# Optimization experiments

Hardware: AMD Instinct MI355X
Metric: run time of the kernel (lower is better)

Reference implementation:

```python
import math
import jax, jax.numpy as jnp
import numpy as np

N_HEADS = 16
D_EMBED = 1024
D_HEAD = D_EMBED // N_HEADS
B, S = 4, 2048


def setup_inputs() -> dict:
    key = jax.random.key(0)
    k1, k2, k3, k4, k5 = jax.random.split(key, 5)
    scale_in = 1.0 / math.sqrt(D_EMBED)
    return {
        "x": jax.random.normal(k1, (B, S, D_EMBED), dtype=jnp.float32),
        "w_in": jax.random.normal(k2, (3 * D_EMBED, D_EMBED), dtype=jnp.float32) * scale_in,
        "b_in": jax.random.normal(k3, (3 * D_EMBED,), dtype=jnp.float32) * 0.02,
        "w_out": jax.random.normal(k4, (D_EMBED, D_EMBED), dtype=jnp.float32) * scale_in,
        "b_out": jax.random.normal(k5, (D_EMBED,), dtype=jnp.float32) * 0.02,
        "causal_mask": 1,
    }


def reference(x, w_in, b_in, w_out, b_out, causal_mask):
    Bn, Sn, D = x.shape
    # fused QKV projection (torch Linear: x @ W.T + b)
    qkv = x @ w_in.T + b_in                       # (B, S, 3D)
    q, k, v = jnp.split(qkv, 3, axis=-1)
    def to_heads(t):
        return t.reshape(Bn, Sn, N_HEADS, D_HEAD).transpose(0, 2, 1, 3)  # (B,H,S,dh)
    q, k, v = to_heads(q), to_heads(k), to_heads(v)
    # manual scaled dot-product attention, full (B,H,S,S) scores
    scores = jnp.einsum("bhqd,bhkd->bhqk", q, k)
    if causal_mask:
        tri = jnp.triu(jnp.ones((Sn, Sn), dtype=bool), k=1)
        scores = jnp.where(tri, -jnp.inf, scores)
    scores = scores / math.sqrt(D_HEAD)
    weights = jax.nn.softmax(scores, axis=-1)
    out = jnp.einsum("bhqk,bhkd->bhqd", weights, v)  # (B,H,S,dh)
    out = out.transpose(0, 2, 1, 3).reshape(Bn, Sn, D)
    return out @ w_out.T + b_out
```

## Files before the change

### kernel.cpp

```cpp
#include <hip/hip_runtime.h>

typedef __bf16 bf16x8 __attribute__((ext_vector_type(8)));
typedef float  f32x4  __attribute__((ext_vector_type(4)));
typedef unsigned int uint;

__device__ inline unsigned short f2bf(float f) {
  union { float f; unsigned int u; } v; v.f = f;
  unsigned int u = v.u;
  unsigned int r = u + 0x7FFF + ((u >> 16) & 1);
  return (unsigned short)(r >> 16);
}

__device__ inline void load_lds16(const unsigned short* g, unsigned short* l) {
  __builtin_amdgcn_global_load_lds(
      (const __attribute__((address_space(1))) uint*)(g),
      (__attribute__((address_space(3))) uint*)(l), 16, 0, 0);
}

__global__ void cvt_f32_bf16(const float* __restrict__ in,
                             unsigned short* __restrict__ out, int n) {
  int i = (blockIdx.x * blockDim.x + threadIdx.x) * 4;
  if (i + 3 < n) {
    float4 f = *reinterpret_cast<const float4*>(in + i);
    ushort4 o;
    o.x = f2bf(f.x); o.y = f2bf(f.y); o.z = f2bf(f.z); o.w = f2bf(f.w);
    *reinterpret_cast<ushort4*>(out + i) = o;
  } else {
    for (; i < n; ++i) out[i] = f2bf(in[i]);
  }
}

template<bool OUT_BF16>
__global__ __launch_bounds__(256) void gemm_bt128(
    const unsigned short* __restrict__ A,
    const unsigned short* __restrict__ B,
    const float* __restrict__ bias,
    void* __restrict__ Cout,
    int M, int N, int K, int ldc)
{
  __shared__ __attribute__((aligned(16))) unsigned short As[128 * 64];
  __shared__ __attribute__((aligned(16))) unsigned short Bs[128 * 64];

  const int t    = threadIdx.x;
  const int wave = t >> 6, lane = t & 63;
  const int l16  = lane & 15, quad = lane >> 4;
  const int wr = wave >> 1, wc = wave & 1;
  const int m0 = blockIdx.y * 128, n0 = blockIdx.x * 128;

  f32x4 acc[4][4] = {};

  for (int k0 = 0; k0 < K; k0 += 64) {
#pragma unroll
    for (int i = 0; i < 4; ++i) {
      int chunk = i * 256 + t;
      int row = chunk >> 3, col = (chunk & 7) * 8;
      load_lds16(A + (size_t)(m0 + row) * K + k0 + col, As + chunk * 8);
    }
#pragma unroll
    for (int i = 0; i < 4; ++i) {
      int chunk = i * 256 + t;
      int row = chunk >> 3, col = (chunk & 7) * 8;
      load_lds16(B + (size_t)(n0 + row) * K + k0 + col, Bs + chunk * 8);
    }
    __syncthreads();
#pragma unroll
    for (int ks = 0; ks < 2; ++ks) {
      bf16x8 af[4], bfr[4];
#pragma unroll
      for (int mt = 0; mt < 4; ++mt)
        af[mt] = *(const bf16x8*)(As + (wr * 64 + mt * 16 + l16) * 64 + ks * 32 + quad * 8);
#pragma unroll
      for (int nt = 0; nt < 4; ++nt)
        bfr[nt] = *(const bf16x8*)(Bs + (wc * 64 + nt * 16 + l16) * 64 + ks * 32 + quad * 8);
#pragma unroll
      for (int mt = 0; mt < 4; ++mt)
#pragma unroll
        for (int nt = 0; nt < 4; ++nt)
          acc[mt][nt] = __builtin_amdgcn_mfma_f32_16x16x32_bf16(af[mt], bfr[nt], acc[mt][nt], 0, 0, 0);
    }
    __syncthreads();
  }

#pragma unroll
  for (int nt = 0; nt < 4; ++nt) {
    int col = n0 + wc * 64 + nt * 16 + l16;
    float bv = bias[col];
#pragma unroll
    for (int mt = 0; mt < 4; ++mt) {
#pragma unroll
      for (int r = 0; r < 4; ++r) {
        int row = m0 + wr * 64 + mt * 16 + quad * 4 + r;
        float v = acc[mt][nt][r] + bv;
        if (OUT_BF16)
          ((unsigned short*)Cout)[(size_t)row * ldc + col] = f2bf(v);
        else
          ((float*)Cout)[(size_t)row * ldc + col] = v;
      }
    }
  }
}

__global__ __launch_bounds__(256) void attn(
    const unsigned short* __restrict__ qkv,
    unsigned short* __restrict__ y,
    const int* __restrict__ flag)
{
  __shared__ __attribute__((aligned(16))) unsigned short Qs[64][72];
  __shared__ __attribute__((aligned(16))) unsigned short Ks[64][72];
  __shared__ __attribute__((aligned(16))) unsigned short VtF[64 * 64];
  __shared__ __attribute__((aligned(16))) unsigned short Ps[64][72];

  const int t    = threadIdx.x;
  const int wave = t >> 6, lane = t & 63;
  const int l16  = lane & 15, quad = lane >> 4;
  const int idx = blockIdx.x;
  const int bh  = idx & 63;
  const int qt  = 31 - (idx >> 6);
  const int b = bh >> 4, h = bh & 15;
  const int causal = flag[0];
  const int q0 = qt * 64;

  const unsigned short* Qg = qkv + (size_t)b * 2048 * 3072 + h * 64;
  const unsigned short* Kg = Qg + 1024;
  const unsigned short* Vg = Qg + 2048;

  {
    int r = t >> 2, c = (t & 3) * 16;
    const unsigned short* src = Qg + (size_t)(q0 + r) * 3072 + c;
    *(uint4*)&Qs[r][c]     = *(const uint4*)src;
    *(uint4*)&Qs[r][c + 8] = *(const uint4*)(src + 8);
  }
  __syncthreads();

  bf16x8 qf[2];
  qf[0] = *(const bf16x8*)&Qs[wave * 16 + l16][quad * 8];
  qf[1] = *(const bf16x8*)&Qs[wave * 16 + l16][32 + quad * 8];

  f32x4 ot[4] = {};
  float l_lane = 0.f;

  const float SCALE = 0.18033688011112042f;
  const int q_glob = q0 + wave * 16 + l16;
  const int jmax = causal ? qt : 31;

  for (int j = 0; j <= jmax; ++j) {
    const int kv0 = j * 64;
    {
      int r = t >> 2, c = (t & 3) * 16;
      const unsigned short* src = Kg + (size_t)(kv0 + r) * 3072 + c;
      *(uint4*)&Ks[r][c]     = *(const uint4*)src;
      *(uint4*)&Ks[r][c + 8] = *(const uint4*)(src + 8);
    }
    {
      int r = t >> 3;
      int c = (t & 7) * 8;
      int g = t & 7;
#pragma unroll
      for (int rr = 0; rr < 64; rr += 32) {
        int kv = r + rr;
        int bk = kv >> 3;
        uint4 vv = *(const uint4*)(Vg + (size_t)(kv0 + kv) * 3072 + c);
        const unsigned short* vs = (const unsigned short*)&vv;
        int base = ((bk ^ g) << 3) + (kv & 7);
#pragma unroll
        for (int i = 0; i < 8; ++i)
          VtF[(c + i) * 64 + base] = vs[i];
      }
    }
    __syncthreads();

    f32x4 st[4] = {};
#pragma unroll
    for (int ks = 0; ks < 2; ++ks) {
#pragma unroll
      for (int mt = 0; mt < 4; ++mt) {
        bf16x8 kf = *(const bf16x8*)&Ks[mt * 16 + l16][ks * 32 + quad * 8];
        st[mt] = __builtin_amdgcn_mfma_f32_16x16x32_bf16(kf, qf[ks], st[mt], 0, 0, 0);
      }
    }

    const bool diag = (causal != 0) && (j == jmax);
#pragma unroll
    for (int mt = 0; mt < 4; ++mt) {
      float p[4];
#pragma unroll
      for (int r = 0; r < 4; ++r) {
        float pv = __builtin_amdgcn_exp2f(st[mt][r] * SCALE);
        if (diag) {
          int kv = kv0 + mt * 16 + quad * 4 + r;
          if (kv > q_glob) pv = 0.f;
        }
        p[r] = pv;
        l_lane += pv;
      }
      uint2 w;
      w.x = (uint)f2bf(p[0]) | ((uint)f2bf(p[1]) << 16);
      w.y = (uint)f2bf(p[2]) | ((uint)f2bf(p[3]) << 16);
      *(uint2*)&Ps[wave * 16 + l16][mt * 16 + quad * 4] = w;
    }
    __threadfence_block();

#pragma unroll
    for (int ks = 0; ks < 2; ++ks) {
      bf16x8 pf = *(const bf16x8*)&Ps[wave * 16 + l16][ks * 32 + quad * 8];
#pragma unroll
      for (int mt = 0; mt < 4; ++mt) {
        int d = mt * 16 + l16;
        int g = (d >> 3) & 7;
        bf16x8 vf = *(const bf16x8*)(VtF + d * 64 + (((ks * 4 + quad) ^ g) << 3));
        ot[mt] = __builtin_amdgcn_mfma_f32_16x16x32_bf16(vf, pf, ot[mt], 0, 0, 0);
      }
    }
    __syncthreads();
  }

  l_lane += __shfl_xor(l_lane, 16);
  l_lane += __shfl_xor(l_lane, 32);
  float inv = 1.f / l_lane;

#pragma unroll
  for (int mt = 0; mt < 4; ++mt) {
    uint2 w;
    w.x = (uint)f2bf(ot[mt][0] * inv) | ((uint)f2bf(ot[mt][1] * inv) << 16);
    w.y = (uint)f2bf(ot[mt][2] * inv) | ((uint)f2bf(ot[mt][3] * inv) << 16);
    *(uint2*)&Ps[wave * 16 + l16][mt * 16 + quad * 4] = w;
  }
  __syncthreads();
  {
    int r = t >> 2, c = (t & 3) * 16;
    size_t base = ((size_t)b * 2048 + q0 + r) * 1024 + h * 64 + c;
    *(uint4*)(y + base)     = *(const uint4*)&Ps[r][c];
    *(uint4*)(y + base + 8) = *(const uint4*)&Ps[r][c + 8];
  }
}

extern "C" void kernel_launch(void* const* d_in, const int* in_sizes, int n_in,
                              void* d_out, int out_size, void* d_ws, size_t ws_size,
                              hipStream_t stream) {
  const float* x     = (const float*)d_in[0];
  const float* w_in  = (const float*)d_in[1];
  const float* b_in  = (const float*)d_in[2];
  const float* w_out = (const float*)d_in[3];
  const float* b_out = (const float*)d_in[4];
  const int*   cmask = (const int*)d_in[5];

  char* ws = (char*)d_ws;
  unsigned short* x_bf     = (unsigned short*)(ws);
  unsigned short* w_in_bf  = (unsigned short*)(ws + 16777216);
  unsigned short* w_out_bf = (unsigned short*)(ws + 23068672);
  unsigned short* qkv_bf   = (unsigned short*)(ws + 25165824);
  unsigned short* y_bf     = (unsigned short*)(ws + 75497472);

  const int n1 = 8192 * 1024, n2 = 3072 * 1024, n3 = 1024 * 1024;
  cvt_f32_bf16<<<dim3((n1 / 4 + 255) / 256), 256, 0, stream>>>(x, x_bf, n1);
  cvt_f32_bf16<<<dim3((n2 / 4 + 255) / 256), 256, 0, stream>>>(w_in, w_in_bf, n2);
  cvt_f32_bf16<<<dim3((n3 / 4 + 255) / 256), 256, 0, stream>>>(w_out, w_out_bf, n3);

  gemm_bt128<true><<<dim3(24, 64), 256, 0, stream>>>(
      x_bf, w_in_bf, b_in, qkv_bf, 8192, 3072, 1024, 3072);

  attn<<<dim3(2048), 256, 0, stream>>>(qkv_bf, y_bf, cmask);

  gemm_bt128<false><<<dim3(8, 64), 256, 0, stream>>>(
      y_bf, w_out_bf, b_out, d_out, 8192, 1024, 1024, 1024);
}
```

Baseline: 294.5 us.

## Prefetch K/V into registers, fold softmax scale into QKV GEMM, reuse Q LDS

The attention kernel now loads the next K/V tile into registers while the current tile is computed, so global load latency overlaps with MFMA work. The softmax scale (1/sqrt(d)·log2e) moves into the QKV GEMM epilogue for the Q columns, which removes a multiply per score. The P buffer reuses the Q shared-memory region to shrink LDS use, the V-transpose swizzle becomes a rotation, and bf16 packing uses a round-half-up perm instruction. The costs are extra registers for the prefetch, a slightly different rounding mode, and Q rounded to bf16 after scaling.

```diff
diff --git a/kernel.cpp b/kernel.cpp
--- a/kernel.cpp
+++ b/kernel.cpp
@@ -9,6 +9,12 @@
   unsigned int u = v.u;
   unsigned int r = u + 0x7FFF + ((u >> 16) & 1);
   return (unsigned short)(r >> 16);
+}
+
+__device__ inline uint pack_bf16_rhu(float a, float b) {
+  uint ua = __builtin_bit_cast(uint, a) + 0x8000u;
+  uint ub = __builtin_bit_cast(uint, b) + 0x8000u;
+  return __builtin_amdgcn_perm(ub, ua, 0x07060302u);
 }
 
 __device__ inline void load_lds16(const unsigned short* g, unsigned short* l) {
@@ -36,7 +42,7 @@
     const unsigned short* __restrict__ B,
     const float* __restrict__ bias,
     void* __restrict__ Cout,
-    int M, int N, int K, int ldc)
+    int M, int N, int K, int ldc, float scale, int ncut)
 {
   __shared__ __attribute__((aligned(16))) unsigned short As[128 * 64];
   __shared__ __attribute__((aligned(16))) unsigned short Bs[128 * 64];
@@ -85,12 +91,13 @@
   for (int nt = 0; nt < 4; ++nt) {
     int col = n0 + wc * 64 + nt * 16 + l16;
     float bv = bias[col];
+    float mlt = (col < ncut) ? scale : 1.0f;
 #pragma unroll
     for (int mt = 0; mt < 4; ++mt) {
 #pragma unroll
       for (int r = 0; r < 4; ++r) {
         int row = m0 + wr * 64 + mt * 16 + quad * 4 + r;
-        float v = acc[mt][nt][r] + bv;
+        float v = (acc[mt][nt][r] + bv) * mlt;
         if (OUT_BF16)
           ((unsigned short*)Cout)[(size_t)row * ldc + col] = f2bf(v);
         else
@@ -108,7 +115,6 @@
   __shared__ __attribute__((aligned(16))) unsigned short Qs[64][72];
   __shared__ __attribute__((aligned(16))) unsigned short Ks[64][72];
   __shared__ __attribute__((aligned(16))) unsigned short VtF[64 * 64];
-  __shared__ __attribute__((aligned(16))) unsigned short Ps[64][72];
 
   const int t    = threadIdx.x;
   const int wave = t >> 6, lane = t & 63;
@@ -131,43 +137,54 @@
     *(uint4*)&Qs[r][c + 8] = *(const uint4*)(src + 8);
   }
   __syncthreads();
-
   bf16x8 qf[2];
   qf[0] = *(const bf16x8*)&Qs[wave * 16 + l16][quad * 8];
   qf[1] = *(const bf16x8*)&Qs[wave * 16 + l16][32 + quad * 8];
+  __syncthreads();
+  unsigned short (*Ps)[72] = Qs;
 
   f32x4 ot[4] = {};
   float l_lane = 0.f;
-
-  const float SCALE = 0.18033688011112042f;
   const int q_glob = q0 + wave * 16 + l16;
   const int jmax = causal ? qt : 31;
+  const int h7 = ((l16 >> 3) + (l16 & 7)) & 7;
+
+  const int kr = t >> 2, kc = (t & 3) * 16;
+  const int vr = t >> 3, vg = t & 7, vc = vg * 8;
+  const int bk0 = vr >> 3, r7 = vr & 7;
+
+  uint4 kreg0, kreg1, vreg0, vreg1;
+  {
+    const unsigned short* src = Kg + (size_t)kr * 3072 + kc;
+    kreg0 = *(const uint4*)src;
+    kreg1 = *(const uint4*)(src + 8);
+    vreg0 = *(const uint4*)(Vg + (size_t)vr * 3072 + vc);
+    vreg1 = *(const uint4*)(Vg + (size_t)(vr + 32) * 3072 + vc);
+  }
 
   for (int j = 0; j <= jmax; ++j) {
-    const int kv0 = j * 64;
+    *(uint4*)&Ks[kr][kc]     = kreg0;
+    *(uint4*)&Ks[kr][kc + 8] = kreg1;
     {
-      int r = t >> 2, c = (t & 3) * 16;
-      const unsigned short* src = Kg + (size_t)(kv0 + r) * 3072 + c;
-      *(uint4*)&Ks[r][c]     = *(const uint4*)src;
-      *(uint4*)&Ks[r][c + 8] = *(const uint4*)(src + 8);
-    }
-    {
-      int r = t >> 3;
-      int c = (t & 7) * 8;
-      int g = t & 7;
-#pragma unroll
-      for (int rr = 0; rr < 64; rr += 32) {
-        int kv = r + rr;
-        int bk = kv >> 3;
-        uint4 vv = *(const uint4*)(Vg + (size_t)(kv0 + kv) * 3072 + c);
-        const unsigned short* vs = (const unsigned short*)&vv;
-        int base = ((bk ^ g) << 3) + (kv & 7);
-#pragma unroll
-        for (int i = 0; i < 8; ++i)
-          VtF[(c + i) * 64 + base] = vs[i];
-      }
-    }
-    __syncthreads();
+      const unsigned short* vs0 = (const unsigned short*)&vreg0;
+      const unsigned short* vs1 = (const unsigned short*)&vreg1;
+#pragma unroll
+      for (int i = 0; i < 8; ++i) {
+        int d = vc + i;
+        VtF[d * 64 + (((bk0     + vg + i) & 7) << 3) + r7] = vs0[i];
+        VtF[d * 64 + (((bk0 + 4 + vg + i) & 7) << 3) + r7] = vs1[i];
+      }
+    }
+    __syncthreads();
+
+    if (j < jmax) {
+      const int kvn = (j + 1) * 64;
+      const unsigned short* src = Kg + (size_t)(kvn + kr) * 3072 + kc;
+      kreg0 = *(const uint4*)src;
+      kreg1 = *(const uint4*)(src + 8);
+      vreg0 = *(const uint4*)(Vg + (size_t)(kvn + vr) * 3072 + vc);
+      vreg1 = *(const uint4*)(Vg + (size_t)(kvn + vr + 32) * 3072 + vc);
+    }
 
     f32x4 st[4] = {};
 #pragma unroll
@@ -179,23 +196,24 @@
       }
     }
 
-    const bool diag = (causal != 0) && (j == jmax);
+    const bool diag = (causal != 0) && (j == qt);
+    const int kv0 = j * 64;
 #pragma unroll
     for (int mt = 0; mt < 4; ++mt) {
       float p[4];
 #pragma unroll
       for (int r = 0; r < 4; ++r) {
-        float pv = __builtin_amdgcn_exp2f(st[mt][r] * SCALE);
+        float pv = __builtin_amdgcn_exp2f(st[mt][r]);
         if (diag) {
           int kv = kv0 + mt * 16 + quad * 4 + r;
           if (kv > q_glob) pv = 0.f;
         }
         p[r] = pv;
-        l_lane += pv;
-      }
+      }
+      l_lane += (p[0] + p[1]) + (p[2] + p[3]);
       uint2 w;
-      w.x = (uint)f2bf(p[0]) | ((uint)f2bf(p[1]) << 16);
-      w.y = (uint)f2bf(p[2]) | ((uint)f2bf(p[3]) << 16);
+      w.x = pack_bf16_rhu(p[0], p[1]);
+      w.y = pack_bf16_rhu(p[2], p[3]);
       *(uint2*)&Ps[wave * 16 + l16][mt * 16 + quad * 4] = w;
     }
     __threadfence_block();
@@ -205,9 +223,8 @@
       bf16x8 pf = *(const bf16x8*)&Ps[wave * 16 + l16][ks * 32 + quad * 8];
 #pragma unroll
       for (int mt = 0; mt < 4; ++mt) {
-        int d = mt * 16 + l16;
-        int g = (d >> 3) & 7;
-        bf16x8 vf = *(const bf16x8*)(VtF + d * 64 + (((ks * 4 + quad) ^ g) << 3));
+        int blk = (ks * 4 + quad + 2 * mt + h7) & 7;
+        bf16x8 vf = *(const bf16x8*)(VtF + (mt * 16 + l16) * 64 + (blk << 3));
         ot[mt] = __builtin_amdgcn_mfma_f32_16x16x32_bf16(vf, pf, ot[mt], 0, 0, 0);
       }
     }
@@ -221,8 +238,8 @@
 #pragma unroll
   for (int mt = 0; mt < 4; ++mt) {
     uint2 w;
-    w.x = (uint)f2bf(ot[mt][0] * inv) | ((uint)f2bf(ot[mt][1] * inv) << 16);
-    w.y = (uint)f2bf(ot[mt][2] * inv) | ((uint)f2bf(ot[mt][3] * inv) << 16);
+    w.x = pack_bf16_rhu(ot[mt][0] * inv, ot[mt][1] * inv);
+    w.y = pack_bf16_rhu(ot[mt][2] * inv, ot[mt][3] * inv);
     *(uint2*)&Ps[wave * 16 + l16][mt * 16 + quad * 4] = w;
   }
   __syncthreads();
@@ -257,10 +274,11 @@
   cvt_f32_bf16<<<dim3((n3 / 4 + 255) / 256), 256, 0, stream>>>(w_out, w_out_bf, n3);
 
   gemm_bt128<true><<<dim3(24, 64), 256, 0, stream>>>(
-      x_bf, w_in_bf, b_in, qkv_bf, 8192, 3072, 1024, 3072);
+      x_bf, w_in_bf, b_in, qkv_bf, 8192, 3072, 1024, 3072,
+      0.18033688011112042f, 1024);
 
   attn<<<dim3(2048), 256, 0, stream>>>(qkv_bf, y_bf, cmask);
 
   gemm_bt128<false><<<dim3(8, 64), 256, 0, stream>>>(
-      y_bf, w_out_bf, b_out, d_out, 8192, 1024, 1024, 1024);
-}
+      y_bf, w_out_bf, b_out, d_out, 8192, 1024, 1024, 1024, 1.0f, 0);
+}
```

Result: faster. 282.2 us (-4.1%).
